# Kernel optimization log

Measured on AMD Instinct MI355X. Metric: run time of the kernel, lower is better.

The kernel has to match this reference:

```python
import jax, jax.numpy as jnp
import numpy as np

N_NODES = 100000
N_EDGES = 1600000
IN_DIM = 192   # n_shapes(64) * n_dims(3)
H1, H2 = 64, 32


def _glorot(key, shape):
    lim = np.sqrt(6.0 / (shape[0] + shape[1])).astype(np.float32)
    return jax.random.uniform(key, shape, jnp.float32, -lim, lim)


def setup_inputs() -> dict:
    key = jax.random.key(0)
    ks = jax.random.split(key, 8)
    verts = jax.random.normal(ks[0], (N_NODES, IN_DIM), jnp.float32)
    edges = jax.random.randint(ks[1], (N_EDGES, 2), 0, N_NODES)
    return {
        "verts": verts,
        "edges": edges,
        "W0_1": _glorot(ks[2], (IN_DIM, H1)),
        "W1_1": _glorot(ks[3], (IN_DIM, H1)),
        "b1": jnp.zeros((H1,), jnp.float32),
        "W0_2": _glorot(ks[4], (H1, H2)),
        "W1_2": _glorot(ks[5], (H1, H2)),
        "b2": jnp.zeros((H2,), jnp.float32),
    }


def cheb_conv(x, src, dst, W0, W1, b, n):
    # ChebConv K=2 with lambda_max=2: L_hat = -D^{-1/2} A D^{-1/2} (zero diagonal)
    deg = jax.ops.segment_sum(jnp.ones(src.shape, x.dtype), src, num_segments=n)
    d_inv = jnp.where(deg > 0, jax.lax.rsqrt(jnp.maximum(deg, 1.0)), 0.0)
    norm = -d_inv[src] * d_inv[dst]                      # [E]
    Tx1 = jax.ops.segment_sum(norm[:, None] * x[src], dst, num_segments=n)  # [n,F]
    return x @ W0 + Tx1 @ W1 + b


def reference(verts, edges, W0_1, W1_1, b1, W0_2, W1_2, b2):
    n = verts.shape[0]
    src, dst = edges[:, 0], edges[:, 1]  # edge_index rows after edges.t()
    x = jax.nn.relu(cheb_conv(verts, src, dst, W0_1, W1_1, b1, n))
    return cheb_conv(x, src, dst, W0_2, W1_2, b2, n)
```

## Files before the change

### kernel.cpp

```cpp
#include <hip/hip_runtime.h>

#define N_NODES 100000
#define N_EDGES 1600000
#define IN_DIM  192
#define H1      64
#define H2      32
#define NBKT    391
#define CAP_D   4608
#define NP1     782
#define NG      1563
#define K1GRID  2345

typedef __attribute__((ext_vector_type(8))) short short8;
typedef __attribute__((ext_vector_type(4))) float f32x4;

__device__ inline short f2bf(float f) {
    union { float f; unsigned u; } v; v.f = f;
    unsigned r = (v.u + 0x7FFFu + ((v.u >> 16) & 1u)) >> 16;
    return (short)r;
}
__device__ inline float bf2f(unsigned short s) {
    union { unsigned u; float f; } v; v.u = ((unsigned)s) << 16;
    return v.f;
}

__global__ __launch_bounds__(1024) void init_kernel(int* __restrict__ bucket_next) {
    int i = threadIdx.x;
    bucket_next[i] = (i & 511) * CAP_D;
}

__global__ __launch_bounds__(256) void prep_w_kernel(
    const float* __restrict__ W0_1, const float* __restrict__ W1_1,
    const float* __restrict__ W0_2, const float* __restrict__ W1_2,
    short* __restrict__ Bt1, short* __restrict__ Bt2) {
    int idx = blockIdx.x * 256 + threadIdx.x;
    if (idx < 128 * IN_DIM) {
        int n = idx / IN_DIM, k = idx % IN_DIM;
        float v = (n < H1) ? W0_1[(size_t)k * H1 + n] : W1_1[(size_t)k * H1 + (n - H1)];
        Bt1[idx] = f2bf(v);
    } else {
        int j = idx - 128 * IN_DIM;
        if (j < 64 * H1) {
            int n = j / H1, k = j % H1;
            float v = (n < H2) ? W0_2[(size_t)k * H2 + n] : W1_2[(size_t)k * H2 + (n - H2)];
            Bt2[j] = f2bf(v);
        }
    }
}

__global__ __launch_bounds__(256) void k1_fused(
    const int* __restrict__ edges, int* __restrict__ bucket_next,
    int* __restrict__ bins_dst, unsigned char* __restrict__ bins_src,
    const float* __restrict__ verts, const short* __restrict__ Bt1,
    const float* __restrict__ b1, short* __restrict__ hbase, short* __restrict__ y1b) {
    __shared__ int cntd[512];
    __shared__ int curd[512];
    __shared__ int cnts[512];
    __shared__ int curs[512];
    int b = blockIdx.x;
    int tid = threadIdx.x;
    if (b % 3 == 0) {
        int p = b / 3;
        cntd[tid] = 0; cntd[tid + 256] = 0;
        cnts[tid] = 0; cnts[tid + 256] = 0;
        __syncthreads();
        int ebase = p * 2048 + tid * 8;
        int2 ed[8]; int bd[8], bs[8];
#pragma unroll
        for (int i = 0; i < 8; ++i) {
            int e = ebase + i;
            if (e < N_EDGES) {
                ed[i] = ((const int2*)edges)[e];
                bd[i] = ed[i].y >> 8;
                bs[i] = ed[i].x >> 8;
                atomicAdd(&cntd[bd[i]], 1);
                atomicAdd(&cnts[bs[i]], 1);
            } else { bd[i] = -1; bs[i] = -1; }
        }
        __syncthreads();
        {
            int c;
            c = cntd[tid];       curd[tid]       = (c > 0) ? atomicAdd(&bucket_next[tid], c) : 0;
            c = cntd[tid + 256]; curd[tid + 256] = (c > 0) ? atomicAdd(&bucket_next[tid + 256], c) : 0;
            c = cnts[tid];       curs[tid]       = (c > 0) ? atomicAdd(&bucket_next[512 + tid], c) : 0;
            c = cnts[tid + 256]; curs[tid + 256] = (c > 0) ? atomicAdd(&bucket_next[512 + tid + 256], c) : 0;
        }
        __syncthreads();
#pragma unroll
        for (int i = 0; i < 8; ++i) {
            if (bd[i] >= 0) {
                int sd = atomicAdd(&curd[bd[i]], 1);
                if (sd < (bd[i] + 1) * CAP_D)
                    bins_dst[sd] = ((ed[i].y & 255) << 17) | ed[i].x;
                int ss = atomicAdd(&curs[bs[i]], 1);
                if (ss < (bs[i] + 1) * CAP_D)
                    bins_src[ss] = (unsigned char)(ed[i].x & 255);
            }
        }
        return;
    }
    int g = b - b / 3 - 1;
    int lane = tid & 63;
    int wave = tid >> 6;
    int rowbase = g * 64 + wave * 16;
    int lr = lane & 15;
    int lk = (lane >> 4) * 8;

    int row = rowbase + lr;
    int rc = (row < N_NODES) ? row : (N_NODES - 1);
    const float* p = verts + (size_t)rc * IN_DIM + lk;
    short8 a[6];
#pragma unroll
    for (int ks = 0; ks < 6; ++ks) {
        f32x4 u0 = *(const f32x4*)(p + ks * 32);
        f32x4 u1 = *(const f32x4*)(p + ks * 32 + 4);
        short8 t;
        t[0] = f2bf(u0[0]); t[1] = f2bf(u0[1]); t[2] = f2bf(u0[2]); t[3] = f2bf(u0[3]);
        t[4] = f2bf(u1[0]); t[5] = f2bf(u1[1]); t[6] = f2bf(u1[2]); t[7] = f2bf(u1[3]);
        a[ks] = t;
    }

    f32x4 acc[8] = {};
#pragma unroll
    for (int cf = 0; cf < 8; ++cf) {
        const short* bp = Bt1 + (size_t)(cf * 16 + lr) * IN_DIM + lk;
#pragma unroll
        for (int ks = 0; ks < 6; ++ks) {
            short8 bb = *(const short8*)(bp + ks * 32);
            acc[cf] = __builtin_amdgcn_mfma_f32_16x16x32_bf16(a[ks], bb, acc[cf], 0, 0, 0);
        }
    }

    int srow = (lane >> 4) * 4;
#pragma unroll
    for (int cf = 0; cf < 8; ++cf) {
        int colc = cf * 16 + lr;
        float bias = (colc < H1) ? b1[colc] : 0.f;
#pragma unroll
        for (int r = 0; r < 4; ++r) {
            int orow = rowbase + srow + r;
            if (orow < N_NODES) {
                float v = acc[cf][r];
                if (colc < H1) hbase[(size_t)orow * H1 + colc] = f2bf(v + bias);
                else           y1b[(size_t)orow * H1 + (colc - H1)] = f2bf(v);
            }
        }
    }
}

__global__ __launch_bounds__(256) void csr_kernel(
    const int* __restrict__ bins_dst, const unsigned char* __restrict__ bins_src,
    const int* __restrict__ bucket_next, float* __restrict__ dinv,
    int* __restrict__ row_beg, int* __restrict__ row_end, int* __restrict__ col) {
    __shared__ int cnt_l[256];
    __shared__ int seg_l[256];
    __shared__ int s[256];
    __shared__ int dcnt[256];
    int b = blockIdx.x;
    int tid = threadIdx.x;
    int beg = b * CAP_D;
    int filld = bucket_next[b] - beg;
    if (filld > CAP_D) filld = CAP_D;
    int fills = bucket_next[512 + b] - beg;
    if (fills > CAP_D) fills = CAP_D;
    cnt_l[tid] = 0;
    dcnt[tid] = 0;
    __syncthreads();
    for (int i = tid; i < filld; i += 256)
        atomicAdd(&cnt_l[bins_dst[beg + i] >> 17], 1);
    for (int i = tid; i < fills; i += 256)
        atomicAdd(&dcnt[bins_src[beg + i]], 1);
    __syncthreads();
    int v = cnt_l[tid];
    s[tid] = v;
    __syncthreads();
    for (int off = 1; off < 256; off <<= 1) {
        int t = (tid >= off) ? s[tid - off] : 0;
        __syncthreads();
        s[tid] += t;
        __syncthreads();
    }
    int excl = s[tid] - v;
    seg_l[tid] = beg + excl;
    int n = b * 256 + tid;
    if (n < N_NODES) {
        row_beg[n] = beg + excl;
        row_end[n] = beg + excl + v;
        int d = dcnt[tid];
        dinv[n] = (d > 0) ? rsqrtf((float)d) : 0.f;
    }
    __syncthreads();
    for (int i = tid; i < filld; i += 256) {
        int w = bins_dst[beg + i];
        int slot = atomicAdd(&seg_l[w >> 17], 1);
        col[slot] = w & 0x1FFFF;
    }
}

__global__ __launch_bounds__(256) void gather1_kernel(
    const int* __restrict__ row_beg, const int* __restrict__ row_end,
    const int* __restrict__ col, const float* __restrict__ dinv,
    const unsigned short* __restrict__ hbase, const unsigned short* __restrict__ y1b,
    short* __restrict__ hb) {
    int n = blockIdx.x * 4 + (threadIdx.x >> 6);
    if (n >= N_NODES) return;
    int lane = threadIdx.x & 63;
    int beg = row_beg[n], end = row_end[n];
    float acc = 0.f;
    int i = beg;
    for (; i + 4 <= end; i += 4) {
        int s0 = col[i], s1 = col[i + 1], s2 = col[i + 2], s3 = col[i + 3];
        float w0 = dinv[s0], w1 = dinv[s1], w2 = dinv[s2], w3 = dinv[s3];
        float v0 = bf2f(y1b[(size_t)s0 * H1 + lane]);
        float v1 = bf2f(y1b[(size_t)s1 * H1 + lane]);
        float v2 = bf2f(y1b[(size_t)s2 * H1 + lane]);
        float v3 = bf2f(y1b[(size_t)s3 * H1 + lane]);
        acc += w0 * v0 + w1 * v1 + w2 * v2 + w3 * v3;
    }
    for (; i < end; ++i) {
        int sc = col[i];
        acc += dinv[sc] * bf2f(y1b[(size_t)sc * H1 + lane]);
    }
    size_t idx = (size_t)n * H1 + lane;
    float hf = bf2f(hbase[idx]) - dinv[n] * acc;
    hb[idx] = f2bf(fmaxf(hf, 0.f));
}

__global__ __launch_bounds__(256) void gemm2_mfma(
    const short* __restrict__ hb, const short* __restrict__ Bt2,
    const float* __restrict__ b2, float* __restrict__ out, short* __restrict__ y2b) {
    int lane = threadIdx.x & 63;
    int wave = threadIdx.x >> 6;
    int rowbase = blockIdx.x * 128 + wave * 32;
    int lr = lane & 15;
    int lk = (lane >> 4) * 8;

    short8 a[2][2];
#pragma unroll
    for (int mr = 0; mr < 2; ++mr) {
        int row = rowbase + mr * 16 + lr;
        int rc = (row < N_NODES) ? row : (N_NODES - 1);
        const short* p = hb + (size_t)rc * H1 + lk;
        a[mr][0] = *(const short8*)(p);
        a[mr][1] = *(const short8*)(p + 32);
    }

    f32x4 acc[2][4] = {};
#pragma unroll
    for (int cf = 0; cf < 4; ++cf) {
        const short* bp = Bt2 + (size_t)(cf * 16 + lr) * H1 + lk;
#pragma unroll
        for (int ks = 0; ks < 2; ++ks) {
            short8 b = *(const short8*)(bp + ks * 32);
            acc[0][cf] = __builtin_amdgcn_mfma_f32_16x16x32_bf16(a[0][ks], b, acc[0][cf], 0, 0, 0);
            acc[1][cf] = __builtin_amdgcn_mfma_f32_16x16x32_bf16(a[1][ks], b, acc[1][cf], 0, 0, 0);
        }
    }

    int srow = (lane >> 4) * 4;
#pragma unroll
    for (int mr = 0; mr < 2; ++mr) {
#pragma unroll
        for (int cf = 0; cf < 4; ++cf) {
            int colc = cf * 16 + lr;
            float bias = (colc < H2) ? b2[colc] : 0.f;
#pragma unroll
            for (int r = 0; r < 4; ++r) {
                int row = rowbase + mr * 16 + srow + r;
                if (row < N_NODES) {
                    float v = acc[mr][cf][r];
                    if (colc < H2) out[(size_t)row * H2 + colc] = v + bias;
                    else           y2b[(size_t)row * H2 + (colc - H2)] = f2bf(v);
                }
            }
        }
    }
}

__global__ __launch_bounds__(256) void gather2_kernel(
    const int* __restrict__ row_beg, const int* __restrict__ row_end,
    const int* __restrict__ col, const float* __restrict__ dinv,
    const unsigned short* __restrict__ y2b, float* __restrict__ out) {
    int wave = (blockIdx.x * 256 + threadIdx.x) >> 6;
    int lane = threadIdx.x & 63;
    int n = wave * 2 + (lane >> 5);
    if (n >= N_NODES) return;
    int c32 = lane & 31;
    int beg = row_beg[n], end = row_end[n];
    float acc = 0.f;
    int i = beg;
    for (; i + 4 <= end; i += 4) {
        int s0 = col[i], s1 = col[i + 1], s2 = col[i + 2], s3 = col[i + 3];
        float w0 = dinv[s0], w1 = dinv[s1], w2 = dinv[s2], w3 = dinv[s3];
        float v0 = bf2f(y2b[(size_t)s0 * H2 + c32]);
        float v1 = bf2f(y2b[(size_t)s1 * H2 + c32]);
        float v2 = bf2f(y2b[(size_t)s2 * H2 + c32]);
        float v3 = bf2f(y2b[(size_t)s3 * H2 + c32]);
        acc += w0 * v0 + w1 * v1 + w2 * v2 + w3 * v3;
    }
    for (; i < end; ++i) {
        int sc = col[i];
        acc += dinv[sc] * bf2f(y2b[(size_t)sc * H2 + c32]);
    }
    size_t idx = (size_t)n * H2 + c32;
    out[idx] = out[idx] - dinv[n] * acc;
}

extern "C" void kernel_launch(void* const* d_in, const int* in_sizes, int n_in,
                              void* d_out, int out_size, void* d_ws, size_t ws_size,
                              hipStream_t stream) {
    const float* verts = (const float*)d_in[0];
    const int*   edges = (const int*)  d_in[1];
    const float* W0_1  = (const float*)d_in[2];
    const float* W1_1  = (const float*)d_in[3];
    const float* b1    = (const float*)d_in[4];
    const float* W0_2  = (const float*)d_in[5];
    const float* W1_2  = (const float*)d_in[6];
    const float* b2    = (const float*)d_in[7];
    float* out = (float*)d_out;

    char* ws = (char*)d_ws;
    auto align256 = [](size_t x) { return (x + 255) & ~(size_t)255; };
    size_t o = 0;
    auto alloc = [&](size_t bytes) { size_t r = o; o = align256(o + bytes); return r; };

    int*   bucket_next = (int*)  (ws + alloc((size_t)1024 * 4));
    int*   bins_dst    = (int*)  (ws + alloc((size_t)NBKT * CAP_D * 4));
    unsigned char* bins_src = (unsigned char*)(ws + alloc((size_t)NBKT * CAP_D));
    int*   col         = (int*)  (ws + alloc((size_t)NBKT * CAP_D * 4));
    int*   row_beg     = (int*)  (ws + alloc((size_t)N_NODES * 4));
    int*   row_end     = (int*)  (ws + alloc((size_t)N_NODES * 4));
    float* dinv        = (float*)(ws + alloc((size_t)N_NODES * 4));
    short* Bt1         = (short*)(ws + alloc((size_t)128 * IN_DIM * 2));
    short* Bt2         = (short*)(ws + alloc((size_t)64 * H1 * 2));
    short* hbase       = (short*)(ws + alloc((size_t)N_NODES * H1 * 2));
    short* y1b         = (short*)(ws + alloc((size_t)N_NODES * H1 * 2));
    short* hb          = (short*)(ws + alloc((size_t)N_NODES * H1 * 2));
    short* y2b         = (short*)(ws + alloc((size_t)N_NODES * H2 * 2));

    init_kernel  <<<1, 1024, 0, stream>>>(bucket_next);
    prep_w_kernel<<<(128 * IN_DIM + 64 * H1 + 255) / 256, 256, 0, stream>>>(W0_1, W1_1, W0_2, W1_2, Bt1, Bt2);

    k1_fused  <<<K1GRID, 256, 0, stream>>>(edges, bucket_next, bins_dst, bins_src,
                                           verts, Bt1, b1, hbase, y1b);
    csr_kernel<<<NBKT, 256, 0, stream>>>(bins_dst, bins_src, bucket_next, dinv,
                                         row_beg, row_end, col);

    gather1_kernel<<<(N_NODES + 3) / 4, 256, 0, stream>>>(row_beg, row_end, col, dinv,
                                                          (const unsigned short*)hbase,
                                                          (const unsigned short*)y1b, hb);
    gemm2_mfma    <<<(N_NODES + 127) / 128, 256, 0, stream>>>(hb, Bt2, b2, out, y2b);
    gather2_kernel<<<(N_NODES + 7) / 8, 256, 0, stream>>>(row_beg, row_end, col, dinv,
                                                          (const unsigned short*)y2b, out);
}
```

Measured before the change: 220.2 us.

## Pre-scale gathered features by source dinv to drop per-edge dinv loads

```diff
diff --git a/kernel.cpp b/kernel.cpp
--- a/kernel.cpp
+++ b/kernel.cpp
@@ -7,8 +7,6 @@
 #define H2      32
 #define NBKT    391
 #define CAP_D   4608
-#define NP1     782
-#define NG      1563
 #define K1GRID  2345
 
 typedef __attribute__((ext_vector_type(8))) short short8;
@@ -151,11 +149,13 @@
 __global__ __launch_bounds__(256) void csr_kernel(
     const int* __restrict__ bins_dst, const unsigned char* __restrict__ bins_src,
     const int* __restrict__ bucket_next, float* __restrict__ dinv,
-    int* __restrict__ row_beg, int* __restrict__ row_end, int* __restrict__ col) {
+    int* __restrict__ row_beg, int* __restrict__ row_end, int* __restrict__ col,
+    const unsigned short* __restrict__ y1b, short* __restrict__ y1s) {
     __shared__ int cnt_l[256];
     __shared__ int seg_l[256];
     __shared__ int s[256];
     __shared__ int dcnt[256];
+    __shared__ float dinv_l[256];
     int b = blockIdx.x;
     int tid = threadIdx.x;
     int beg = b * CAP_D;
@@ -183,11 +183,13 @@
     int excl = s[tid] - v;
     seg_l[tid] = beg + excl;
     int n = b * 256 + tid;
+    int d = dcnt[tid];
+    float dv = (d > 0) ? rsqrtf((float)d) : 0.f;
+    dinv_l[tid] = dv;
     if (n < N_NODES) {
         row_beg[n] = beg + excl;
         row_end[n] = beg + excl + v;
-        int d = dcnt[tid];
-        dinv[n] = (d > 0) ? rsqrtf((float)d) : 0.f;
+        dinv[n] = dv;
     }
     __syncthreads();
     for (int i = tid; i < filld; i += 256) {
@@ -195,12 +197,24 @@
         int slot = atomicAdd(&seg_l[w >> 17], 1);
         col[slot] = w & 0x1FFFF;
     }
+    int nb = b * 256;
+    int nmax = N_NODES - nb; if (nmax > 256) nmax = 256;
+    for (int idx = tid; idx < nmax * 8; idx += 256) {
+        int r = idx >> 3, j = idx & 7;
+        float w = dinv_l[r];
+        size_t off = (size_t)(nb + r) * H1 + j * 8;
+        short8 vv = *(const short8*)&y1b[off];
+        short8 o;
+#pragma unroll
+        for (int q = 0; q < 8; ++q) o[q] = f2bf(w * bf2f((unsigned short)vv[q]));
+        *(short8*)&y1s[off] = o;
+    }
 }
 
 __global__ __launch_bounds__(256) void gather1_kernel(
     const int* __restrict__ row_beg, const int* __restrict__ row_end,
     const int* __restrict__ col, const float* __restrict__ dinv,
-    const unsigned short* __restrict__ hbase, const unsigned short* __restrict__ y1b,
+    const unsigned short* __restrict__ hbase, const unsigned short* __restrict__ y1s,
     short* __restrict__ hb) {
     int n = blockIdx.x * 4 + (threadIdx.x >> 6);
     if (n >= N_NODES) return;
@@ -208,19 +222,29 @@
     int beg = row_beg[n], end = row_end[n];
     float acc = 0.f;
     int i = beg;
+    for (; i + 8 <= end; i += 8) {
+        int s0 = col[i], s1 = col[i + 1], s2 = col[i + 2], s3 = col[i + 3];
+        int s4 = col[i + 4], s5 = col[i + 5], s6 = col[i + 6], s7 = col[i + 7];
+        float v0 = bf2f(y1s[(size_t)s0 * H1 + lane]);
+        float v1 = bf2f(y1s[(size_t)s1 * H1 + lane]);
+        float v2 = bf2f(y1s[(size_t)s2 * H1 + lane]);
+        float v3 = bf2f(y1s[(size_t)s3 * H1 + lane]);
+        float v4 = bf2f(y1s[(size_t)s4 * H1 + lane]);
+        float v5 = bf2f(y1s[(size_t)s5 * H1 + lane]);
+        float v6 = bf2f(y1s[(size_t)s6 * H1 + lane]);
+        float v7 = bf2f(y1s[(size_t)s7 * H1 + lane]);
+        acc += ((v0 + v1) + (v2 + v3)) + ((v4 + v5) + (v6 + v7));
+    }
     for (; i + 4 <= end; i += 4) {
         int s0 = col[i], s1 = col[i + 1], s2 = col[i + 2], s3 = col[i + 3];
-        float w0 = dinv[s0], w1 = dinv[s1], w2 = dinv[s2], w3 = dinv[s3];
-        float v0 = bf2f(y1b[(size_t)s0 * H1 + lane]);
-        float v1 = bf2f(y1b[(size_t)s1 * H1 + lane]);
-        float v2 = bf2f(y1b[(size_t)s2 * H1 + lane]);
-        float v3 = bf2f(y1b[(size_t)s3 * H1 + lane]);
-        acc += w0 * v0 + w1 * v1 + w2 * v2 + w3 * v3;
-    }
-    for (; i < end; ++i) {
-        int sc = col[i];
-        acc += dinv[sc] * bf2f(y1b[(size_t)sc * H1 + lane]);
-    }
+        float v0 = bf2f(y1s[(size_t)s0 * H1 + lane]);
+        float v1 = bf2f(y1s[(size_t)s1 * H1 + lane]);
+        float v2 = bf2f(y1s[(size_t)s2 * H1 + lane]);
+        float v3 = bf2f(y1s[(size_t)s3 * H1 + lane]);
+        acc += (v0 + v1) + (v2 + v3);
+    }
+    for (; i < end; ++i)
+        acc += bf2f(y1s[(size_t)col[i] * H1 + lane]);
     size_t idx = (size_t)n * H1 + lane;
     float hf = bf2f(hbase[idx]) - dinv[n] * acc;
     hb[idx] = f2bf(fmaxf(hf, 0.f));
@@ -228,7 +252,8 @@
 
 __global__ __launch_bounds__(256) void gemm2_mfma(
     const short* __restrict__ hb, const short* __restrict__ Bt2,
-    const float* __restrict__ b2, float* __restrict__ out, short* __restrict__ y2b) {
+    const float* __restrict__ b2, const float* __restrict__ dinv,
+    float* __restrict__ out, short* __restrict__ y2s) {
     int lane = threadIdx.x & 63;
     int wave = threadIdx.x >> 6;
     int rowbase = blockIdx.x * 128 + wave * 32;
@@ -270,7 +295,7 @@
                 if (row < N_NODES) {
                     float v = acc[mr][cf][r];
                     if (colc < H2) out[(size_t)row * H2 + colc] = v + bias;
-                    else           y2b[(size_t)row * H2 + (colc - H2)] = f2bf(v);
+                    else           y2s[(size_t)row * H2 + (colc - H2)] = f2bf(dinv[row] * v);
                 }
             }
         }
@@ -280,7 +305,7 @@
 __global__ __launch_bounds__(256) void gather2_kernel(
     const int* __restrict__ row_beg, const int* __restrict__ row_end,
     const int* __restrict__ col, const float* __restrict__ dinv,
-    const unsigned short* __restrict__ y2b, float* __restrict__ out) {
+    const unsigned short* __restrict__ y2s, float* __restrict__ out) {
     int wave = (blockIdx.x * 256 + threadIdx.x) >> 6;
     int lane = threadIdx.x & 63;
     int n = wave * 2 + (lane >> 5);
@@ -289,19 +314,29 @@
     int beg = row_beg[n], end = row_end[n];
     float acc = 0.f;
     int i = beg;
+    for (; i + 8 <= end; i += 8) {
+        int s0 = col[i], s1 = col[i + 1], s2 = col[i + 2], s3 = col[i + 3];
+        int s4 = col[i + 4], s5 = col[i + 5], s6 = col[i + 6], s7 = col[i + 7];
+        float v0 = bf2f(y2s[(size_t)s0 * H2 + c32]);
+        float v1 = bf2f(y2s[(size_t)s1 * H2 + c32]);
+        float v2 = bf2f(y2s[(size_t)s2 * H2 + c32]);
+        float v3 = bf2f(y2s[(size_t)s3 * H2 + c32]);
+        float v4 = bf2f(y2s[(size_t)s4 * H2 + c32]);
+        float v5 = bf2f(y2s[(size_t)s5 * H2 + c32]);
+        float v6 = bf2f(y2s[(size_t)s6 * H2 + c32]);
+        float v7 = bf2f(y2s[(size_t)s7 * H2 + c32]);
+        acc += ((v0 + v1) + (v2 + v3)) + ((v4 + v5) + (v6 + v7));
+    }
     for (; i + 4 <= end; i += 4) {
         int s0 = col[i], s1 = col[i + 1], s2 = col[i + 2], s3 = col[i + 3];
-        float w0 = dinv[s0], w1 = dinv[s1], w2 = dinv[s2], w3 = dinv[s3];
-        float v0 = bf2f(y2b[(size_t)s0 * H2 + c32]);
-        float v1 = bf2f(y2b[(size_t)s1 * H2 + c32]);
-        float v2 = bf2f(y2b[(size_t)s2 * H2 + c32]);
-        float v3 = bf2f(y2b[(size_t)s3 * H2 + c32]);
-        acc += w0 * v0 + w1 * v1 + w2 * v2 + w3 * v3;
-    }
-    for (; i < end; ++i) {
-        int sc = col[i];
-        acc += dinv[sc] * bf2f(y2b[(size_t)sc * H2 + c32]);
-    }
+        float v0 = bf2f(y2s[(size_t)s0 * H2 + c32]);
+        float v1 = bf2f(y2s[(size_t)s1 * H2 + c32]);
+        float v2 = bf2f(y2s[(size_t)s2 * H2 + c32]);
+        float v3 = bf2f(y2s[(size_t)s3 * H2 + c32]);
+        acc += (v0 + v1) + (v2 + v3);
+    }
+    for (; i < end; ++i)
+        acc += bf2f(y2s[(size_t)col[i] * H2 + c32]);
     size_t idx = (size_t)n * H2 + c32;
     out[idx] = out[idx] - dinv[n] * acc;
 }
@@ -335,8 +370,9 @@
     short* Bt2         = (short*)(ws + alloc((size_t)64 * H1 * 2));
     short* hbase       = (short*)(ws + alloc((size_t)N_NODES * H1 * 2));
     short* y1b         = (short*)(ws + alloc((size_t)N_NODES * H1 * 2));
+    short* y1s         = (short*)(ws + alloc((size_t)N_NODES * H1 * 2));
     short* hb          = (short*)(ws + alloc((size_t)N_NODES * H1 * 2));
-    short* y2b         = (short*)(ws + alloc((size_t)N_NODES * H2 * 2));
+    short* y2s         = (short*)(ws + alloc((size_t)N_NODES * H2 * 2));
 
     init_kernel  <<<1, 1024, 0, stream>>>(bucket_next);
     prep_w_kernel<<<(128 * IN_DIM + 64 * H1 + 255) / 256, 256, 0, stream>>>(W0_1, W1_1, W0_2, W1_2, Bt1, Bt2);
@@ -344,12 +380,13 @@
     k1_fused  <<<K1GRID, 256, 0, stream>>>(edges, bucket_next, bins_dst, bins_src,
                                            verts, Bt1, b1, hbase, y1b);
     csr_kernel<<<NBKT, 256, 0, stream>>>(bins_dst, bins_src, bucket_next, dinv,
-                                         row_beg, row_end, col);
+                                         row_beg, row_end, col,
+                                         (const unsigned short*)y1b, y1s);
 
     gather1_kernel<<<(N_NODES + 3) / 4, 256, 0, stream>>>(row_beg, row_end, col, dinv,
                                                           (const unsigned short*)hbase,
-                                                          (const unsigned short*)y1b, hb);
-    gemm2_mfma    <<<(N_NODES + 127) / 128, 256, 0, stream>>>(hb, Bt2, b2, out, y2b);
+                                                          (const unsigned short*)y1s, hb);
+    gemm2_mfma    <<<(N_NODES + 127) / 128, 256, 0, stream>>>(hb, Bt2, b2, dinv, out, y2s);
     gather2_kernel<<<(N_NODES + 7) / 8, 256, 0, stream>>>(row_beg, row_end, col, dinv,
-                                                          (const unsigned short*)y2b, out);
-}
+                                                          (const unsigned short*)y2s, out);
+}
```

Result: faster. 206.4 us (-6.2%).
